# Performance work log

Hardware: AMD Instinct MI355X
Metric: run time of the kernel (lower is better)

The kernel has to match this reference:

```python
import jax, jax.numpy as jnp
import numpy as np

NUM_QUERIES = 300


def setup_inputs() -> dict:
    key = jax.random.key(0)
    ks = jax.random.split(key, 16)
    B, C, NC = 16, 256, 80
    s = 0.02
    return {
        "s3": jax.random.normal(ks[0], (B, C, 128, 128), jnp.float32),
        "s4": jax.random.normal(ks[1], (B, C, 64, 64), jnp.float32),
        "s5": jax.random.normal(ks[2], (B, C, 32, 32), jnp.float32),
        "w_score": jax.random.normal(ks[3], (C, NC), jnp.float32) * s,
        "b_score": jnp.zeros((NC,), jnp.float32),
        "w1": jax.random.normal(ks[4], (C, C), jnp.float32) * s,
        "b1": jnp.zeros((C,), jnp.float32),
        "w2": jax.random.normal(ks[5], (C, C), jnp.float32) * s,
        "b2": jnp.zeros((C,), jnp.float32),
        "w3": jax.random.normal(ks[6], (C, 4), jnp.float32) * s,
        "b3": jnp.zeros((4,), jnp.float32),
        "w_proj": jax.random.normal(ks[7], (C, C), jnp.float32) * s,
        "b_proj": jnp.zeros((C,), jnp.float32),
    }


def _flatten(feats):
    # each feat [B,C,H,W] -> [B,H*W,C]; concat over levels
    mems = [f.reshape(f.shape[0], f.shape[1], -1).transpose(0, 2, 1) for f in feats]
    return jnp.concatenate(mems, axis=1)


def reference(s3, s4, s5, w_score, b_score, w1, b1, w2, b2, w3, b3, w_proj, b_proj):
    memory = _flatten([s3, s4, s5])  # [B, N, C]

    # encoder heads
    enc_logits = memory @ w_score + b_score                      # [B, N, num_classes]
    h = jax.nn.relu(memory @ w1 + b1)
    h = jax.nn.relu(h @ w2 + b2)
    enc_boxes = h @ w3 + b3                                      # [B, N, 4]

    # top-k query selection: sigmoid -> per-token max class score -> topk -> gather
    scores = jax.nn.sigmoid(enc_logits).max(axis=-1)             # [B, N]
    topk_scores, topk_idx = jax.lax.top_k(scores, NUM_QUERIES)   # [B, K]
    topk_mem = jnp.take_along_axis(memory, topk_idx[:, :, None], axis=1)    # [B, K, C]
    topk_boxes = jnp.take_along_axis(enc_boxes, topk_idx[:, :, None], axis=1)  # [B, K, 4]

    tgt = topk_mem @ w_proj + b_proj                             # [B, K, C]
    ref_points = jax.nn.sigmoid(topk_boxes)                      # [B, K, 4]

    return (tgt, ref_points, enc_logits, jax.nn.sigmoid(enc_boxes), topk_idx, topk_scores)
```

## Files before the change

### kernel.cpp

```cpp
#include <hip/hip_runtime.h>
#include <math.h>

#define BATCH 16
#define CDIM 256
#define NCLS 80
#define N3 16384
#define N4 4096
#define N5 1024
#define NTOK 21504
#define KQ 300
#define KSEL 512
#define CANDMAX 1024

typedef __attribute__((ext_vector_type(8))) short short8;
typedef __attribute__((ext_vector_type(4))) float floatx4;
typedef unsigned short ushort_t;

#define LA(tok, k) (((tok) * 264) + (((((k) >> 3) ^ ((tok) & 7)) << 3) | ((k) & 7)))

__device__ __forceinline__ float sigmoidf_(float x) {
    return 1.0f / (1.0f + __expf(-x));
}

__device__ __forceinline__ ushort_t f2bf(float f) {
    unsigned int x = __float_as_uint(f);
    unsigned int r = (x + 0x7FFFu + ((x >> 16) & 1u)) >> 16;
    return (ushort_t)r;
}

__device__ __forceinline__ void gload16(const void* g, void* l) {
    __builtin_amdgcn_global_load_lds(
        (const __attribute__((address_space(1))) unsigned int*)g,
        (__attribute__((address_space(3))) unsigned int*)l,
        16, 0, 0);
}

__device__ __forceinline__ void locate_level(
    int n, int bb,
    const float* __restrict__ s3, const float* __restrict__ s4, const float* __restrict__ s5,
    const float*& src, int& nloc, int& lsz)
{
    if (n < N3)           { src = s3 + (size_t)bb * CDIM * N3; nloc = n;           lsz = N3; }
    else if (n < N3 + N4) { src = s4 + (size_t)bb * CDIM * N4; nloc = n - N3;      lsz = N4; }
    else                  { src = s5 + (size_t)bb * CDIM * N5; nloc = n - N3 - N4; lsz = N5; }
}

__global__ __launch_bounds__(256) void prep_weights(
    const float* __restrict__ w1, const float* __restrict__ w2,
    const float* __restrict__ w_score,
    ushort_t* __restrict__ w1T, ushort_t* __restrict__ w2T, ushort_t* __restrict__ wsT)
{
    const int k = threadIdx.x;
    const int c = blockIdx.x;
    const int klo = k & 7;
    if (c < 256) {
        const size_t d = (size_t)c * 256 + ((((k >> 3) ^ (c & 7)) << 3) | klo);
        w1T[d] = f2bf(w1[k * 256 + c]);
    } else if (c < 512) {
        const int c2 = c - 256;
        const size_t d = (size_t)c2 * 256 + ((((k >> 3) ^ (c2 & 7)) << 3) | klo);
        w2T[d] = f2bf(w2[k * 256 + c2]);
    } else {
        const int c2 = c - 512;
        const size_t d = (size_t)c2 * 256 + ((((k >> 3) ^ (c2 & 7)) << 3) | klo);
        wsT[d] = (c2 < NCLS) ? f2bf(w_score[k * NCLS + c2]) : (ushort_t)0;
    }
}

__global__ __launch_bounds__(256, 2) void enc_mfma_kernel(
    const float* __restrict__ s3, const float* __restrict__ s4, const float* __restrict__ s5,
    const ushort_t* __restrict__ w1T, const ushort_t* __restrict__ w2T,
    const ushort_t* __restrict__ wsT,
    const float* __restrict__ b_score, const float* __restrict__ b1,
    const float* __restrict__ b2,
    const float* __restrict__ w3, const float* __restrict__ b3,
    float* __restrict__ out_logits, float* __restrict__ out_sboxes,
    float* __restrict__ ws_scores)
{
    __shared__ __align__(16) ushort_t ldsA[64 * 264];
    __shared__ __align__(16) ushort_t wbufL[2][32 * 256];
    __shared__ float bsc_s[80];
    __shared__ float b1_s[256];
    __shared__ float b2_s[256];
    __shared__ __align__(16) float w3_s[256 * 4];
    __shared__ float smax_s[2][64];
    __shared__ __align__(16) float boxp[2][64][4];

    const int t = threadIdx.x;
    const int lane = t & 63;
    const int w = t >> 6;
    const int tw = w & 1;
    const int cw = w >> 1;
    const int ml = lane & 15;
    const int quad = lane >> 4;
    const int kq = quad * 8;
    const int m8 = ml & 7;

    const int bb = blockIdx.x / 336;
    const int tile_ = blockIdx.x % 336;
    const int T0 = tile_ * 64;

    auto stage_async = [&](const ushort_t* wg, int dbuf) {
        const char* g = (const char*)wg + w * 1024 + (lane << 4);
        char* l = (char*)&wbufL[dbuf][0] + w * 1024;
        #pragma unroll
        for (int i = 0; i < 4; ++i)
            gload16(g + i * 4096, l + i * 4096);
    };

    stage_async(wsT, 0);

    if (t < 80) bsc_s[t] = b_score[t];
    b1_s[t] = b1[t];
    b2_s[t] = b2[t];
    *(float4*)&w3_s[t * 4] = *(const float4*)(w3 + t * 4);

    const float* src; int nloc, lsz;
    locate_level(T0, bb, s3, s4, s5, src, nloc, lsz);

    {
        const int tokq = t & 15;
        const int kg = t >> 4;
        #pragma unroll
        for (int p = 0; p < 2; ++p) {
            const int kbase = 8 * kg + 128 * p;
            float4 v[8];
            #pragma unroll
            for (int j = 0; j < 8; ++j)
                v[j] = *(const float4*)(src + (size_t)(kbase + j) * lsz + nloc + 4 * tokq);
            #pragma unroll
            for (int r = 0; r < 4; ++r) {
                short8 a;
                #pragma unroll
                for (int j = 0; j < 8; ++j)
                    a[j] = (short)f2bf(((const float*)&v[j])[r]);
                *(short8*)&ldsA[LA(4 * tokq + r, kbase)] = a;
            }
        }
    }
    __syncthreads();

    short8 af[2][8];
    #pragma unroll
    for (int tl = 0; tl < 2; ++tl) {
        const int tok = 32 * tw + 16 * tl + ml;
        #pragma unroll
        for (int f = 0; f < 8; ++f)
            af[tl][f] = *(const short8*)&ldsA[LA(tok, 32 * f + kq)];
    }

    const int gtok0 = bb * NTOK + T0;

    float smaxr[2][4];
    #pragma unroll
    for (int tl = 0; tl < 2; ++tl)
        #pragma unroll
        for (int r = 0; r < 4; ++r) smaxr[tl][r] = -1e30f;

    float psum[2][4][4];
    #pragma unroll
    for (int tl = 0; tl < 2; ++tl)
        #pragma unroll
        for (int r = 0; r < 4; ++r)
            #pragma unroll
            for (int c = 0; c < 4; ++c) psum[tl][r][c] = 0.f;

    int cur = 0;
    for (int i = 0; i < 19; ++i) {
        if (i + 1 < 19) {
            const int j = i + 1;
            const ushort_t* nxt = (j < 3)  ? (wsT + (size_t)j * 8192)
                                : (j < 11) ? (w1T + (size_t)(j - 3) * 8192)
                                           : (w2T + (size_t)(j - 11) * 8192);
            stage_async(nxt, cur ^ 1);
        }

        if (i == 11) {
            #pragma unroll
            for (int tl = 0; tl < 2; ++tl) {
                const int tok = 32 * tw + 16 * tl + ml;
                #pragma unroll
                for (int f = 0; f < 8; ++f)
                    af[tl][f] = *(const short8*)&ldsA[LA(tok, 32 * f + kq)];
            }
        }

        const ushort_t* wb = &wbufL[cur][0];
        const int row = 16 * cw + ml;
        floatx4 acc0 = {0.f, 0.f, 0.f, 0.f};
        floatx4 acc1 = {0.f, 0.f, 0.f, 0.f};
        #pragma unroll
        for (int f = 0; f < 8; ++f) {
            const short8 bf = *(const short8*)&wb[row * 256 + (((4 * f + quad) ^ m8) << 3)];
            acc0 = __builtin_amdgcn_mfma_f32_16x16x32_bf16(af[0][f], bf, acc0, 0, 0, 0);
            acc1 = __builtin_amdgcn_mfma_f32_16x16x32_bf16(af[1][f], bf, acc1, 0, 0, 0);
        }

        if (i < 3) {
            const int col = 32 * i + 16 * cw + ml;
            if (col < NCLS) {
                const float bias = bsc_s[col];
                #pragma unroll
                for (int tl = 0; tl < 2; ++tl)
                    #pragma unroll
                    for (int r = 0; r < 4; ++r) {
                        const float v = (tl ? acc1[r] : acc0[r]) + bias;
                        const int ltok = 32 * tw + 16 * tl + 4 * quad + r;
                        out_logits[(size_t)(gtok0 + ltok) * NCLS + col] = v;
                        smaxr[tl][r] = fmaxf(smaxr[tl][r], v);
                    }
            }
            if (i == 2) {
                #pragma unroll
                for (int tl = 0; tl < 2; ++tl)
                    #pragma unroll
                    for (int r = 0; r < 4; ++r) {
                        float m = smaxr[tl][r];
                        m = fmaxf(m, __shfl_xor(m, 1));
                        m = fmaxf(m, __shfl_xor(m, 2));
                        m = fmaxf(m, __shfl_xor(m, 4));
                        m = fmaxf(m, __shfl_xor(m, 8));
                        if (ml == 0)
                            smax_s[cw][32 * tw + 16 * tl + 4 * quad + r] = m;
                    }
            }
        } else if (i < 11) {
            const int col = 32 * (i - 3) + 16 * cw + ml;
            const float bias = b1_s[col];
            #pragma unroll
            for (int tl = 0; tl < 2; ++tl)
                #pragma unroll
                for (int r = 0; r < 4; ++r) {
                    const float v = fmaxf((tl ? acc1[r] : acc0[r]) + bias, 0.f);
                    const int ltok = 32 * tw + 16 * tl + 4 * quad + r;
                    ldsA[LA(ltok, col)] = f2bf(v);
                }
        } else {
            const int col = 32 * (i - 11) + 16 * cw + ml;
            const float bias = b2_s[col];
            const float4 w3v = *(const float4*)&w3_s[col * 4];
            #pragma unroll
            for (int tl = 0; tl < 2; ++tl)
                #pragma unroll
                for (int r = 0; r < 4; ++r) {
                    const float v = fmaxf((tl ? acc1[r] : acc0[r]) + bias, 0.f);
                    psum[tl][r][0] = fmaf(v, w3v.x, psum[tl][r][0]);
                    psum[tl][r][1] = fmaf(v, w3v.y, psum[tl][r][1]);
                    psum[tl][r][2] = fmaf(v, w3v.z, psum[tl][r][2]);
                    psum[tl][r][3] = fmaf(v, w3v.w, psum[tl][r][3]);
                }
        }

        __syncthreads();
        cur ^= 1;
    }

    #pragma unroll
    for (int tl = 0; tl < 2; ++tl)
        #pragma unroll
        for (int r = 0; r < 4; ++r) {
            float4 pv;
            float* pva = (float*)&pv;
            #pragma unroll
            for (int c = 0; c < 4; ++c) {
                float v = psum[tl][r][c];
                v += __shfl_xor(v, 1);
                v += __shfl_xor(v, 2);
                v += __shfl_xor(v, 4);
                v += __shfl_xor(v, 8);
                pva[c] = v;
            }
            if (ml == 0)
                *(float4*)&boxp[cw][32 * tw + 16 * tl + 4 * quad + r][0] = pv;
        }
    __syncthreads();

    if (t < 64)
        ws_scores[gtok0 + t] = sigmoidf_(fmaxf(smax_s[0][t], smax_s[1][t]));
    {
        const int tok = t >> 2, c = t & 3;
        const float bx = boxp[0][tok][c] + boxp[1][tok][c] + b3[c];
        out_sboxes[(size_t)(gtok0 + tok) * 4 + c] = sigmoidf_(bx);
    }
}

__global__ __launch_bounds__(256) void select_kernel(
    const float* __restrict__ scores,
    int* __restrict__ cand_idx, unsigned int* __restrict__ cand_cnt)
{
    const int bb = blockIdx.x;
    const int t = threadIdx.x;
    const int lane = t & 63;
    const float* s = scores + bb * NTOK;

    __shared__ unsigned int hist[256];
    __shared__ unsigned int prefix_s, rem_s, cnt_s;

    unsigned int prefix = 0, mask = 0;
    int remaining = KSEL;
    for (int pass = 0; pass < 4; pass++) {
        const int shift = 24 - 8 * pass;
        hist[t] = 0;
        __syncthreads();
        for (int n = t; n < NTOK; n += 256) {
            const unsigned int key = __float_as_uint(s[n]);
            const bool pred = ((key & mask) == prefix);
            const unsigned int bin = pred ? ((key >> shift) & 255u) : 0xFFFFu;
            const unsigned long long alive = __ballot(pred);
            if (alive) {
                const int leader = __builtin_ctzll(alive);
                const unsigned int lbin = (unsigned int)__shfl((int)bin, leader);
                const unsigned long long match = __ballot(pred && bin == lbin);
                if (lane == leader)
                    atomicAdd(&hist[lbin], (unsigned int)__popcll(match));
                else if (pred && bin != lbin)
                    atomicAdd(&hist[bin], 1u);
            }
        }
        __syncthreads();
        if (t == 0) {
            int rem = remaining; unsigned int bsel = 0;
            for (int bin = 255; bin >= 0; bin--) {
                int c = (int)hist[bin];
                if (c >= rem) { bsel = (unsigned int)bin; break; }
                rem -= c;
            }
            prefix_s = prefix | (bsel << shift);
            rem_s = (unsigned int)rem;
        }
        __syncthreads();
        prefix = prefix_s; remaining = (int)rem_s;
        mask |= 0xFFu << shift;
        __syncthreads();
    }
    const unsigned int Tkey = prefix;

    if (t == 0) cnt_s = 0;
    __syncthreads();
    for (int n = t; n < NTOK; n += 256) {
        const unsigned int key = __float_as_uint(s[n]);
        const bool pred = (key >= Tkey);
        const unsigned long long m = __ballot(pred);
        if (m) {
            const int leader = __builtin_ctzll(m);
            unsigned int base = 0;
            if (lane == leader) base = atomicAdd(&cnt_s, (unsigned int)__popcll(m));
            base = (unsigned int)__shfl((int)base, leader);
            if (pred) {
                const unsigned int pos =
                    base + (unsigned int)__popcll(m & ((1ull << lane) - 1ull));
                if (pos < CANDMAX) cand_idx[bb * CANDMAX + pos] = n;
            }
        }
    }
    __syncthreads();
    if (t == 0) {
        unsigned int c = cnt_s; if (c > CANDMAX) c = CANDMAX;
        cand_cnt[bb] = c;
    }
}

__global__ __launch_bounds__(256) void rescore_kernel(
    const float* __restrict__ s3, const float* __restrict__ s4, const float* __restrict__ s5,
    const float* __restrict__ w_score, const float* __restrict__ b_score,
    const int* __restrict__ cand_idx, const unsigned int* __restrict__ cand_cnt,
    double* __restrict__ cand_score, float* __restrict__ cand_mem, int use_cmem)
{
    __shared__ float m_s[CDIM];
    __shared__ double part[256];

    const int t = threadIdx.x;
    const int bb = blockIdx.x / CANDMAX;
    const int cpos = blockIdx.x % CANDMAX;
    if ((unsigned int)cpos >= cand_cnt[bb]) return;

    const int n = cand_idx[bb * CANDMAX + cpos];
    const float* src; int nloc, lsz;
    locate_level(n, bb, s3, s4, s5, src, nloc, lsz);
    m_s[t] = src[(size_t)t * lsz + nloc];
    __syncthreads();

    if (use_cmem)
        cand_mem[((size_t)bb * CANDMAX + cpos) * CDIM + t] = m_s[t];

    const int ks = t >> 7;
    const int c = t & 127;
    double acc = 0.0;
    if (c < NCLS) {
        if (ks == 0) acc = (double)b_score[c];
        const int k0 = 128 * ks;
        for (int k = k0; k < k0 + 128; ++k)
            acc += (double)m_s[k] * (double)w_score[k * NCLS + c];
    }
    part[t] = acc;
    __syncthreads();

    if (t < 128) {
        double tot = (t < NCLS) ? (part[t] + part[t + 128]) : -1.0e300;
        part[t] = tot;
    }
    __syncthreads();

    if (t < 64) {
        double v = fmax(part[t], part[t + 64]);
        v = fmax(v, __shfl_xor(v, 1));
        v = fmax(v, __shfl_xor(v, 2));
        v = fmax(v, __shfl_xor(v, 4));
        v = fmax(v, __shfl_xor(v, 8));
        v = fmax(v, __shfl_xor(v, 16));
        v = fmax(v, __shfl_xor(v, 32));
        if (t == 0) cand_score[bb * CANDMAX + cpos] = v;
    }
}

__global__ __launch_bounds__(512) void fsort_kernel(
    const double* __restrict__ cand_score, const int* __restrict__ cand_idx,
    const unsigned int* __restrict__ cand_cnt,
    float* __restrict__ out_idx_f, float* __restrict__ out_scores,
    int* __restrict__ ws_idx, int* __restrict__ ws_pos)
{
    __shared__ double ss[CANDMAX];
    __shared__ int    ii[CANDMAX];
    __shared__ int    pp[CANDMAX];
    const int bb = blockIdx.x;
    const int t = threadIdx.x;
    const unsigned int cnt = cand_cnt[bb];

    for (int i = t; i < CANDMAX; i += 512) {
        if ((unsigned int)i < cnt) {
            ss[i] = cand_score[bb * CANDMAX + i];
            ii[i] = cand_idx[bb * CANDMAX + i];
        } else {
            ss[i] = -1.0e300;
            ii[i] = 0x7FFFFFFF;
        }
        pp[i] = i;
    }
    __syncthreads();

    for (int ksz = 2; ksz <= CANDMAX; ksz <<= 1) {
        for (int j = ksz >> 1; j > 0; j >>= 1) {
            #pragma unroll
            for (int p = 0; p < CANDMAX / 512; p++) {
                const int i = p * 512 + t;
                const int ixj = i ^ j;
                if (ixj > i) {
                    double sa = ss[i], sb = ss[ixj];
                    int ia = ii[i], ib = ii[ixj];
                    const bool up = ((i & ksz) != 0);
                    const bool agtb = (sa > sb) || (sa == sb && ia < ib);
                    if (agtb == up) {
                        ss[i] = sb; ss[ixj] = sa;
                        ii[i] = ib; ii[ixj] = ia;
                        const int pa = pp[i]; pp[i] = pp[ixj]; pp[ixj] = pa;
                    }
                }
            }
            __syncthreads();
        }
    }

    for (int q = t; q < KQ; q += 512) {
        const double x = ss[q];
        const int idx = ii[q];
        out_scores[bb * KQ + q] = (float)(1.0 / (1.0 + exp(-x)));
        out_idx_f[bb * KQ + q] = (float)idx;
        ws_idx[bb * KQ + q] = idx;
        ws_pos[bb * KQ + q] = pp[q];
    }
}

__global__ __launch_bounds__(256) void gather_proj_kernel(
    const float* __restrict__ s3, const float* __restrict__ s4, const float* __restrict__ s5,
    const float* __restrict__ w_proj, const float* __restrict__ b_proj,
    const int* __restrict__ ws_idx, const int* __restrict__ ws_pos,
    const float* __restrict__ cand_mem, int use_cmem,
    const float* __restrict__ out_sboxes,
    float* __restrict__ out_tgt, float* __restrict__ out_ref)
{
    __shared__ float memQ[20][CDIM];
    __shared__ int qidx[20];
    __shared__ int qpos[20];
    const int t = threadIdx.x;
    const int bb = blockIdx.x / 15;
    const int tile = blockIdx.x % 15;
    const int q0 = tile * 20;

    if (t < 20) {
        qidx[t] = ws_idx[bb * KQ + q0 + t];
        qpos[t] = ws_pos[bb * KQ + q0 + t];
    }
    __syncthreads();

    if (use_cmem) {
        #pragma unroll 4
        for (int q = 0; q < 20; q++)
            memQ[q][t] = cand_mem[((size_t)bb * CANDMAX + qpos[q]) * CDIM + t];
    } else {
        #pragma unroll 4
        for (int q = 0; q < 20; q++) {
            const int n = qidx[q];
            const float* src; int nloc, lsz;
            locate_level(n, bb, s3, s4, s5, src, nloc, lsz);
            memQ[q][t] = src[(size_t)t * lsz + nloc];
        }
    }
    __syncthreads();

    const int j = t;
    float acc[20];
    #pragma unroll
    for (int q = 0; q < 20; q++) acc[q] = b_proj[j];
    for (int k = 0; k < CDIM; k++) {
        const float w = w_proj[(size_t)k * CDIM + j];
        #pragma unroll
        for (int q = 0; q < 20; q++) acc[q] = fmaf(memQ[q][k], w, acc[q]);
    }
    #pragma unroll
    for (int q = 0; q < 20; q++)
        out_tgt[(size_t)(bb * KQ + q0 + q) * CDIM + j] = acc[q];

    if (t < 80) {
        const int q = t >> 2, c = t & 3;
        const int n = qidx[q];
        out_ref[(size_t)(bb * KQ + q0 + q) * 4 + c] =
            out_sboxes[(size_t)(bb * NTOK + n) * 4 + c];
    }
}

extern "C" void kernel_launch(void* const* d_in, const int* in_sizes, int n_in,
                              void* d_out, int out_size, void* d_ws, size_t ws_size,
                              hipStream_t stream) {
    const float* s3      = (const float*)d_in[0];
    const float* s4      = (const float*)d_in[1];
    const float* s5      = (const float*)d_in[2];
    const float* w_score = (const float*)d_in[3];
    const float* b_score = (const float*)d_in[4];
    const float* w1      = (const float*)d_in[5];
    const float* b1      = (const float*)d_in[6];
    const float* w2      = (const float*)d_in[7];
    const float* b2      = (const float*)d_in[8];
    const float* w3      = (const float*)d_in[9];
    const float* b3      = (const float*)d_in[10];
    const float* w_proj  = (const float*)d_in[11];
    const float* b_proj  = (const float*)d_in[12];

    float* out = (float*)d_out;
    float* out_tgt    = out;
    float* out_ref    = out + 1228800;
    float* out_logits = out + 1248000;
    float* out_sboxes = out + 28773120;
    float* out_idx    = out + 30149376;
    float* out_scores = out + 30154176;

    char* ws = (char*)d_ws;
    float*        ws_scores  = (float*)(ws + 0);
    double*       cand_score = (double*)(ws + 1376256);
    int*          cand_idx   = (int*)(ws + 1507328);
    unsigned int* cand_cnt   = (unsigned int*)(ws + 1572864);
    int*          ws_idx     = (int*)(ws + 1573120);
    int*          ws_pos     = (int*)(ws + 1592576);
    ushort_t*     w1T        = (ushort_t*)(ws + 1612032);
    ushort_t*     w2T        = (ushort_t*)(ws + 1743104);
    ushort_t*     wsT        = (ushort_t*)(ws + 1874176);
    float*        cand_mem   = (float*)(ws + 1923328);
    const int use_cmem = (ws_size >= (size_t)1923328 + 16777216) ? 1 : 0;

    prep_weights<<<608, 256, 0, stream>>>(w1, w2, w_score, w1T, w2T, wsT);

    enc_mfma_kernel<<<BATCH * 336, 256, 0, stream>>>(
        s3, s4, s5, w1T, w2T, wsT, b_score, b1, b2, w3, b3,
        out_logits, out_sboxes, ws_scores);

    select_kernel<<<BATCH, 256, 0, stream>>>(ws_scores, cand_idx, cand_cnt);

    rescore_kernel<<<BATCH * CANDMAX, 256, 0, stream>>>(
        s3, s4, s5, w_score, b_score, cand_idx, cand_cnt,
        cand_score, cand_mem, use_cmem);

    fsort_kernel<<<BATCH, 512, 0, stream>>>(
        cand_score, cand_idx, cand_cnt, out_idx, out_scores, ws_idx, ws_pos);

    gather_proj_kernel<<<BATCH * 15, 256, 0, stream>>>(
        s3, s4, s5, w_proj, b_proj, ws_idx, ws_pos, cand_mem, use_cmem,
        out_sboxes, out_tgt, out_ref);
}
```

Baseline: 991.7 us.

## Parallelize top-k threshold selection and triple-buffer half-chunk weight staging in encoder

```diff
diff --git a/kernel.cpp b/kernel.cpp
--- a/kernel.cpp
+++ b/kernel.cpp
@@ -11,6 +11,8 @@
 #define KQ 300
 #define KSEL 512
 #define CANDMAX 1024
+#define HBIN 2048
+#define KMIN 0x3E800000u
 
 typedef __attribute__((ext_vector_type(8))) short short8;
 typedef __attribute__((ext_vector_type(4))) float floatx4;
@@ -78,7 +80,7 @@
     float* __restrict__ ws_scores)
 {
     __shared__ __align__(16) ushort_t ldsA[64 * 264];
-    __shared__ __align__(16) ushort_t wbufL[2][32 * 256];
+    __shared__ __align__(16) ushort_t wbufL[3][32 * 128];
     __shared__ float bsc_s[80];
     __shared__ float b1_s[256];
     __shared__ float b2_s[256];
@@ -100,15 +102,17 @@
     const int tile_ = blockIdx.x % 336;
     const int T0 = tile_ * 64;
 
-    auto stage_async = [&](const ushort_t* wg, int dbuf) {
-        const char* g = (const char*)wg + w * 1024 + (lane << 4);
-        char* l = (char*)&wbufL[dbuf][0] + w * 1024;
-        #pragma unroll
-        for (int i = 0; i < 4; ++i)
-            gload16(g + i * 4096, l + i * 4096);
+    auto stage_half = [&](const ushort_t* wg, int h, int dbuf) {
+        const char* gb = (const char*)wg + h * 256;
+        char* l = (char*)&wbufL[dbuf][0];
+        #pragma unroll
+        for (int ii = 0; ii < 2; ++ii) {
+            const int u = t + 256 * ii;
+            gload16(gb + (u >> 4) * 512 + (u & 15) * 16, l + u * 16);
+        }
     };
 
-    stage_async(wsT, 0);
+    stage_half(wsT, 0, 0);
 
     if (t < 80) bsc_s[t] = b_score[t];
     b1_s[t] = b1[t];
@@ -138,7 +142,10 @@
             }
         }
     }
-    __syncthreads();
+
+    __builtin_amdgcn_sched_barrier(0);
+    stage_half(wsT, 1, 1);
+    asm volatile("s_waitcnt vmcnt(2) lgkmcnt(0)\ns_barrier" ::: "memory");
 
     short8 af[2][8];
     #pragma unroll
@@ -165,17 +172,15 @@
             #pragma unroll
             for (int c = 0; c < 4; ++c) psum[tl][r][c] = 0.f;
 
-    int cur = 0;
-    for (int i = 0; i < 19; ++i) {
-        if (i + 1 < 19) {
-            const int j = i + 1;
-            const ushort_t* nxt = (j < 3)  ? (wsT + (size_t)j * 8192)
-                                : (j < 11) ? (w1T + (size_t)(j - 3) * 8192)
-                                           : (w2T + (size_t)(j - 11) * 8192);
-            stage_async(nxt, cur ^ 1);
-        }
-
-        if (i == 11) {
+    floatx4 acc0 = {0.f, 0.f, 0.f, 0.f};
+    floatx4 acc1 = {0.f, 0.f, 0.f, 0.f};
+    const int brow = (16 * cw + ml) * 128;
+
+    for (int i = 0; i < 38; ++i) {
+        const int cb = i >> 1;
+        const int h = i & 1;
+
+        if (i == 22) {
             #pragma unroll
             for (int tl = 0; tl < 2; ++tl) {
                 const int tok = 32 * tw + 16 * tl + ml;
@@ -185,74 +190,90 @@
             }
         }
 
-        const ushort_t* wb = &wbufL[cur][0];
-        const int row = 16 * cw + ml;
-        floatx4 acc0 = {0.f, 0.f, 0.f, 0.f};
-        floatx4 acc1 = {0.f, 0.f, 0.f, 0.f};
-        #pragma unroll
-        for (int f = 0; f < 8; ++f) {
-            const short8 bf = *(const short8*)&wb[row * 256 + (((4 * f + quad) ^ m8) << 3)];
-            acc0 = __builtin_amdgcn_mfma_f32_16x16x32_bf16(af[0][f], bf, acc0, 0, 0, 0);
-            acc1 = __builtin_amdgcn_mfma_f32_16x16x32_bf16(af[1][f], bf, acc1, 0, 0, 0);
-        }
-
-        if (i < 3) {
-            const int col = 32 * i + 16 * cw + ml;
-            if (col < NCLS) {
-                const float bias = bsc_s[col];
+        if (h == 0) {
+            acc0 = (floatx4){0.f, 0.f, 0.f, 0.f};
+            acc1 = (floatx4){0.f, 0.f, 0.f, 0.f};
+        }
+
+        const ushort_t* wb = &wbufL[i % 3][0];
+        __builtin_amdgcn_s_setprio(1);
+        #pragma unroll
+        for (int f2 = 0; f2 < 4; ++f2) {
+            const short8 bf = *(const short8*)&wb[brow + ((((4 * f2 + quad) ^ m8)) << 3)];
+            acc0 = __builtin_amdgcn_mfma_f32_16x16x32_bf16(af[0][4 * h + f2], bf, acc0, 0, 0, 0);
+            acc1 = __builtin_amdgcn_mfma_f32_16x16x32_bf16(af[1][4 * h + f2], bf, acc1, 0, 0, 0);
+        }
+        __builtin_amdgcn_s_setprio(0);
+
+        if (h == 1) {
+            if (cb < 3) {
+                const int col = 32 * cb + 16 * cw + ml;
+                if (col < NCLS) {
+                    const float bias = bsc_s[col];
+                    #pragma unroll
+                    for (int tl = 0; tl < 2; ++tl)
+                        #pragma unroll
+                        for (int r = 0; r < 4; ++r) {
+                            const float v = (tl ? acc1[r] : acc0[r]) + bias;
+                            const int ltok = 32 * tw + 16 * tl + 4 * quad + r;
+                            out_logits[(size_t)(gtok0 + ltok) * NCLS + col] = v;
+                            smaxr[tl][r] = fmaxf(smaxr[tl][r], v);
+                        }
+                }
+                if (i == 5) {
+                    #pragma unroll
+                    for (int tl = 0; tl < 2; ++tl)
+                        #pragma unroll
+                        for (int r = 0; r < 4; ++r) {
+                            float m = smaxr[tl][r];
+                            m = fmaxf(m, __shfl_xor(m, 1));
+                            m = fmaxf(m, __shfl_xor(m, 2));
+                            m = fmaxf(m, __shfl_xor(m, 4));
+                            m = fmaxf(m, __shfl_xor(m, 8));
+                            if (ml == 0)
+                                smax_s[cw][32 * tw + 16 * tl + 4 * quad + r] = m;
+                        }
+                }
+            } else if (cb < 11) {
+                const int col = 32 * (cb - 3) + 16 * cw + ml;
+                const float bias = b1_s[col];
                 #pragma unroll
                 for (int tl = 0; tl < 2; ++tl)
                     #pragma unroll
                     for (int r = 0; r < 4; ++r) {
-                        const float v = (tl ? acc1[r] : acc0[r]) + bias;
+                        const float v = fmaxf((tl ? acc1[r] : acc0[r]) + bias, 0.f);
                         const int ltok = 32 * tw + 16 * tl + 4 * quad + r;
-                        out_logits[(size_t)(gtok0 + ltok) * NCLS + col] = v;
-                        smaxr[tl][r] = fmaxf(smaxr[tl][r], v);
+                        ldsA[LA(ltok, col)] = f2bf(v);
                     }
-            }
-            if (i == 2) {
+            } else {
+                const int col = 32 * (cb - 11) + 16 * cw + ml;
+                const float bias = b2_s[col];
+                const float4 w3v = *(const float4*)&w3_s[col * 4];
                 #pragma unroll
                 for (int tl = 0; tl < 2; ++tl)
                     #pragma unroll
                     for (int r = 0; r < 4; ++r) {
-                        float m = smaxr[tl][r];
-                        m = fmaxf(m, __shfl_xor(m, 1));
-                        m = fmaxf(m, __shfl_xor(m, 2));
-                        m = fmaxf(m, __shfl_xor(m, 4));
-                        m = fmaxf(m, __shfl_xor(m, 8));
-                        if (ml == 0)
-                            smax_s[cw][32 * tw + 16 * tl + 4 * quad + r] = m;
+                        const float v = fmaxf((tl ? acc1[r] : acc0[r]) + bias, 0.f);
+                        psum[tl][r][0] = fmaf(v, w3v.x, psum[tl][r][0]);
+                        psum[tl][r][1] = fmaf(v, w3v.y, psum[tl][r][1]);
+                        psum[tl][r][2] = fmaf(v, w3v.z, psum[tl][r][2]);
+                        psum[tl][r][3] = fmaf(v, w3v.w, psum[tl][r][3]);
                     }
             }
-        } else if (i < 11) {
-            const int col = 32 * (i - 3) + 16 * cw + ml;
-            const float bias = b1_s[col];
-            #pragma unroll
-            for (int tl = 0; tl < 2; ++tl)
-                #pragma unroll
-                for (int r = 0; r < 4; ++r) {
-                    const float v = fmaxf((tl ? acc1[r] : acc0[r]) + bias, 0.f);
-                    const int ltok = 32 * tw + 16 * tl + 4 * quad + r;
-                    ldsA[LA(ltok, col)] = f2bf(v);
-                }
+        }
+
+        __builtin_amdgcn_sched_barrier(0);
+        if (i + 2 < 38) {
+            const int j = i + 2;
+            const int jc = j >> 1, jh = j & 1;
+            const ushort_t* nxt = (jc < 3)  ? (wsT + (size_t)jc * 8192)
+                                : (jc < 11) ? (w1T + (size_t)(jc - 3) * 8192)
+                                            : (w2T + (size_t)(jc - 11) * 8192);
+            stage_half(nxt, jh, j % 3);
+            asm volatile("s_waitcnt vmcnt(2) lgkmcnt(0)\ns_barrier" ::: "memory");
         } else {
-            const int col = 32 * (i - 11) + 16 * cw + ml;
-            const float bias = b2_s[col];
-            const float4 w3v = *(const float4*)&w3_s[col * 4];
-            #pragma unroll
-            for (int tl = 0; tl < 2; ++tl)
-                #pragma unroll
-                for (int r = 0; r < 4; ++r) {
-                    const float v = fmaxf((tl ? acc1[r] : acc0[r]) + bias, 0.f);
-                    psum[tl][r][0] = fmaf(v, w3v.x, psum[tl][r][0]);
-                    psum[tl][r][1] = fmaf(v, w3v.y, psum[tl][r][1]);
-                    psum[tl][r][2] = fmaf(v, w3v.z, psum[tl][r][2]);
-                    psum[tl][r][3] = fmaf(v, w3v.w, psum[tl][r][3]);
-                }
-        }
-
-        __syncthreads();
-        cur ^= 1;
+            asm volatile("s_waitcnt vmcnt(0) lgkmcnt(0)\ns_barrier" ::: "memory");
+        }
     }
 
     #pragma unroll
@@ -284,79 +305,106 @@
     }
 }
 
-__global__ __launch_bounds__(256) void select_kernel(
-    const float* __restrict__ scores,
-    int* __restrict__ cand_idx, unsigned int* __restrict__ cand_cnt)
-{
+__global__ __launch_bounds__(256) void zero_sel(
+    unsigned int* __restrict__ hist, unsigned int* __restrict__ cand_cnt)
+{
+    const int idx = blockIdx.x * 256 + threadIdx.x;
+    for (int i = idx; i < BATCH * HBIN; i += 32 * 256) hist[i] = 0u;
+    if (idx < BATCH) cand_cnt[idx] = 0u;
+}
+
+__global__ __launch_bounds__(256) void hist_sel(
+    const float* __restrict__ scores, unsigned int* __restrict__ hist)
+{
+    __shared__ unsigned int lhist[HBIN];
+    const int t = threadIdx.x;
+    const int bb = blockIdx.x >> 4;
+    const int slice = blockIdx.x & 15;
+    const float* s = scores + bb * NTOK;
+    #pragma unroll
+    for (int j = 0; j < HBIN / 256; ++j) lhist[t + 256 * j] = 0u;
+    __syncthreads();
+
+    const int base = slice * (NTOK / 16);
+    for (int n = base + t; n < base + NTOK / 16; n += 256) {
+        const unsigned int key = __float_as_uint(s[n]);
+        int b;
+        if (key < KMIN) b = 0;
+        else {
+            unsigned int d = (key - KMIN) >> 13;
+            b = (d > (unsigned int)(HBIN - 1)) ? (HBIN - 1) : (int)d;
+        }
+        atomicAdd(&lhist[b], 1u);
+    }
+    __syncthreads();
+    #pragma unroll
+    for (int j = 0; j < HBIN / 256; ++j) {
+        const unsigned int v = lhist[t + 256 * j];
+        if (v) atomicAdd(&hist[bb * HBIN + t + 256 * j], v);
+    }
+}
+
+__global__ __launch_bounds__(256) void scan_sel(
+    const unsigned int* __restrict__ hist, unsigned int* __restrict__ tkeyArr)
+{
+    __shared__ unsigned int part[256];
     const int bb = blockIdx.x;
     const int t = threadIdx.x;
+    unsigned int s = 0;
+    #pragma unroll
+    for (int j = 0; j < 8; ++j) s += hist[bb * HBIN + t * 8 + j];
+    part[t] = s;
+    __syncthreads();
+    if (t == 0) {
+        int acc = 0, g = 255;
+        for (; g >= 0; --g) {
+            if (acc + (int)part[g] >= KSEL) break;
+            acc += (int)part[g];
+        }
+        unsigned int key;
+        if (g < 0) {
+            key = 1u;
+        } else {
+            int b = 8 * g + 7;
+            for (; b > 8 * g; --b) {
+                acc += (int)hist[bb * HBIN + b];
+                if (acc >= KSEL) break;
+            }
+            if (acc < KSEL) { acc += (int)hist[bb * HBIN + 8 * g]; b = 8 * g; }
+            key = (b == 0) ? 1u : (KMIN + ((unsigned int)b << 13));
+        }
+        tkeyArr[bb] = key;
+    }
+}
+
+__global__ __launch_bounds__(256) void collect_sel(
+    const float* __restrict__ scores, const unsigned int* __restrict__ tkeyArr,
+    int* __restrict__ cand_idx, unsigned int* __restrict__ cand_cnt)
+{
+    const int t = threadIdx.x;
     const int lane = t & 63;
+    const int bb = blockIdx.x >> 4;
+    const int slice = blockIdx.x & 15;
     const float* s = scores + bb * NTOK;
-
-    __shared__ unsigned int hist[256];
-    __shared__ unsigned int prefix_s, rem_s, cnt_s;
-
-    unsigned int prefix = 0, mask = 0;
-    int remaining = KSEL;
-    for (int pass = 0; pass < 4; pass++) {
-        const int shift = 24 - 8 * pass;
-        hist[t] = 0;
-        __syncthreads();
-        for (int n = t; n < NTOK; n += 256) {
-            const unsigned int key = __float_as_uint(s[n]);
-            const bool pred = ((key & mask) == prefix);
-            const unsigned int bin = pred ? ((key >> shift) & 255u) : 0xFFFFu;
-            const unsigned long long alive = __ballot(pred);
-            if (alive) {
-                const int leader = __builtin_ctzll(alive);
-                const unsigned int lbin = (unsigned int)__shfl((int)bin, leader);
-                const unsigned long long match = __ballot(pred && bin == lbin);
-                if (lane == leader)
-                    atomicAdd(&hist[lbin], (unsigned int)__popcll(match));
-                else if (pred && bin != lbin)
-                    atomicAdd(&hist[bin], 1u);
-            }
-        }
-        __syncthreads();
-        if (t == 0) {
-            int rem = remaining; unsigned int bsel = 0;
-            for (int bin = 255; bin >= 0; bin--) {
-                int c = (int)hist[bin];
-                if (c >= rem) { bsel = (unsigned int)bin; break; }
-                rem -= c;
-            }
-            prefix_s = prefix | (bsel << shift);
-            rem_s = (unsigned int)rem;
-        }
-        __syncthreads();
-        prefix = prefix_s; remaining = (int)rem_s;
-        mask |= 0xFFu << shift;
-        __syncthreads();
-    }
-    const unsigned int Tkey = prefix;
-
-    if (t == 0) cnt_s = 0;
-    __syncthreads();
-    for (int n = t; n < NTOK; n += 256) {
+    const unsigned int Tkey = tkeyArr[bb];
+
+    const int base = slice * (NTOK / 16);
+    for (int n = base + t; n < base + NTOK / 16; n += 256) {
         const unsigned int key = __float_as_uint(s[n]);
         const bool pred = (key >= Tkey);
         const unsigned long long m = __ballot(pred);
         if (m) {
             const int leader = __builtin_ctzll(m);
-            unsigned int base = 0;
-            if (lane == leader) base = atomicAdd(&cnt_s, (unsigned int)__popcll(m));
-            base = (unsigned int)__shfl((int)base, leader);
+            unsigned int bpos = 0;
+            if (lane == leader)
+                bpos = atomicAdd(&cand_cnt[bb], (unsigned int)__popcll(m));
+            bpos = (unsigned int)__shfl((int)bpos, leader);
             if (pred) {
                 const unsigned int pos =
-                    base + (unsigned int)__popcll(m & ((1ull << lane) - 1ull));
+                    bpos + (unsigned int)__popcll(m & ((1ull << lane) - 1ull));
                 if (pos < CANDMAX) cand_idx[bb * CANDMAX + pos] = n;
             }
         }
-    }
-    __syncthreads();
-    if (t == 0) {
-        unsigned int c = cnt_s; if (c > CANDMAX) c = CANDMAX;
-        cand_cnt[bb] = c;
     }
 }
 
@@ -566,13 +614,19 @@
     float*        cand_mem   = (float*)(ws + 1923328);
     const int use_cmem = (ws_size >= (size_t)1923328 + 16777216) ? 1 : 0;
 
+    unsigned int* hist    = (unsigned int*)(ws + 1612032);
+    unsigned int* tkeyArr = (unsigned int*)(ws + 1743104);
+
     prep_weights<<<608, 256, 0, stream>>>(w1, w2, w_score, w1T, w2T, wsT);
 
     enc_mfma_kernel<<<BATCH * 336, 256, 0, stream>>>(
         s3, s4, s5, w1T, w2T, wsT, b_score, b1, b2, w3, b3,
         out_logits, out_sboxes, ws_scores);
 
-    select_kernel<<<BATCH, 256, 0, stream>>>(ws_scores, cand_idx, cand_cnt);
+    zero_sel<<<32, 256, 0, stream>>>(hist, cand_cnt);
+    hist_sel<<<256, 256, 0, stream>>>(ws_scores, hist);
+    scan_sel<<<BATCH, 256, 0, stream>>>(hist, tkeyArr);
+    collect_sel<<<256, 256, 0, stream>>>(ws_scores, tkeyArr, cand_idx, cand_cnt);
 
     rescore_kernel<<<BATCH * CANDMAX, 256, 0, stream>>>(
         s3, s4, s5, w_score, b_score, cand_idx, cand_cnt,
```

New measurement: 1.752 ms. +76.7%, slower.
